# Kernel optimization log

Measured on AMD Instinct MI355X. Metric: run time of the kernel, lower is better.

Reference implementation:

```python
import jax, jax.numpy as jnp
import numpy as np

C = 64; NB_ERB = 32; NB_DF = 96; EMB = 256; KT = 2
LSNR_SCALE = 50.0; LSNR_OFFSET = -15.0

def _conv2d(x, w, b, stride=(1, 1)):
    # NCHW conv; freq padding 1, no temporal padding (causal ring buffer handles time)
    out = jax.lax.conv_general_dilated(
        x, w, window_strides=stride, padding=((0, 0), (1, 1)),
        dimension_numbers=('NCHW', 'OIHW', 'NCHW'))
    return out + b[None, :, None, None]


def setup_inputs() -> dict:
    key = jax.random.key(0)
    ks = jax.random.split(key, 32)
    n = lambda i, shape, s=0.05: jax.random.normal(ks[i], shape, dtype=jnp.float32) * s
    return {
        'feat_erb': n(0, (1, 1, 1, NB_ERB), 1.0),
        'feat_spec': n(1, (1, 2, 1, NB_DF), 1.0),
        'buf_erb0': n(2, (1, 1, KT - 1, NB_ERB), 1.0),
        'buf_df0': n(3, (1, 2, KT - 1, NB_DF), 1.0),
        'h_enc': n(4, (1, 1, EMB), 1.0),
        'W_erb0': n(5, (C, 1, KT, 3)), 'b_erb0': n(6, (C,)),
        'W_erb1': n(7, (C, C, 1, 3)), 'b_erb1': n(8, (C,)),
        'W_erb2': n(9, (C, C, 1, 3)), 'b_erb2': n(10, (C,)),
        'W_erb3': n(11, (C, C, 1, 3)), 'b_erb3': n(12, (C,)),
        'W_df0': n(13, (C, 2, KT, 3)), 'b_df0': n(14, (C,)),
        'W_df1': n(15, (C, C, 1, 3)), 'b_df1': n(16, (C,)),
        'W_dffc': n(17, (EMB, C * (NB_DF // 2))), 'b_dffc': n(18, (EMB,)),
        'W_ih': n(19, (3 * EMB, EMB)), 'b_ih': n(20, (3 * EMB,)),
        'W_hh': n(21, (3 * EMB, EMB)), 'b_hh': n(22, (3 * EMB,)),
        'W_lsnr': n(23, (1, EMB)), 'b_lsnr': n(24, (1,)),
    }


def reference(feat_erb, feat_spec, buf_erb0, buf_df0, h_enc,
              W_erb0, b_erb0, W_erb1, b_erb1, W_erb2, b_erb2, W_erb3, b_erb3,
              W_df0, b_df0, W_df1, b_df1, W_dffc, b_dffc,
              W_ih, b_ih, W_hh, b_hh, W_lsnr, b_lsnr):
    relu = jax.nn.relu
    # ERB path: causal conv via explicit ring buffer
    ctx_erb = jnp.concatenate([buf_erb0, feat_erb], axis=2)     # [1,1,KT,32]
    e0 = relu(_conv2d(ctx_erb, W_erb0, b_erb0))                 # [1,C,1,32]
    buf_erb0_new = ctx_erb[:, :, 1:, :]
    e1 = relu(_conv2d(e0, W_erb1, b_erb1, stride=(1, 2)))       # [1,C,1,16]
    e2 = relu(_conv2d(e1, W_erb2, b_erb2, stride=(1, 2)))       # [1,C,1,8]
    e3 = relu(_conv2d(e2, W_erb3, b_erb3, stride=(1, 2)))       # [1,C,1,4]
    # DF path
    ctx_df = jnp.concatenate([buf_df0, feat_spec], axis=2)      # [1,2,KT,96]
    c0 = relu(_conv2d(ctx_df, W_df0, b_df0))                    # [1,C,1,96]
    buf_df0_new = ctx_df[:, :, 1:, :]
    c1 = relu(_conv2d(c0, W_df1, b_df1, stride=(1, 2)))         # [1,C,1,48]
    c1f = jnp.transpose(c1, (0, 2, 3, 1)).reshape(1, 1, -1)     # [1,1,48*C]
    cemb = relu(c1f @ W_dffc.T + b_dffc)                        # [1,1,EMB]
    emb_raw = jnp.transpose(e3, (0, 2, 3, 1)).reshape(1, 1, -1) # [1,1,EMB]
    emb_raw = emb_raw + cemb                                    # combine = add
    # Single-layer GRU step (torch gate semantics)
    x2 = emb_raw[:, 0]                                          # [1,EMB]
    h2 = h_enc[0]                                               # [1,EMB]
    gi = x2 @ W_ih.T + b_ih
    gh = h2 @ W_hh.T + b_hh
    ir, iz, inn = jnp.split(gi, 3, axis=-1)
    hr, hz, hn = jnp.split(gh, 3, axis=-1)
    r = jax.nn.sigmoid(ir + hr)
    z = jax.nn.sigmoid(iz + hz)
    ng = jnp.tanh(inn + r * hn)
    h_new = (1.0 - z) * ng + z * h2                             # [1,EMB]
    emb = h_new[:, None, :]                                     # [1,1,EMB]
    h_enc_new = h_new[None]                                     # [1,1,EMB]
    lsnr = (jax.nn.sigmoid(emb @ W_lsnr.T + b_lsnr) * LSNR_SCALE + LSNR_OFFSET).reshape(1)
    return (e0, e1, e2, e3, emb, c0, lsnr, buf_erb0_new, buf_df0_new, h_enc_new)
```

## Files before the change

### kernel.cpp

```cpp
#include <hip/hip_runtime.h>
#include <math.h>

#define C 64
#define NB_ERB 32
#define NB_DF 96
#define EMB 256

#define OUT_E0      0
#define OUT_E1      2048
#define OUT_E2      3072
#define OUT_E3      3584
#define OUT_EMB     3840
#define OUT_C0      4096
#define OUT_LSNR    10240
#define OUT_BUF_ERB 10241
#define OUT_BUF_DF  10273
#define OUT_HENC    10465

#define WS_GH   0
#define WS_PART 768

static __device__ __forceinline__ float sigm(float x) {
    return 1.0f / (1.0f + expf(-x));
}

__global__ __launch_bounds__(256) void k1(
    const float* __restrict__ feat_erb, const float* __restrict__ feat_spec,
    const float* __restrict__ buf_erb0, const float* __restrict__ buf_df0,
    const float* __restrict__ h_enc,
    const float* __restrict__ W_erb0, const float* __restrict__ b_erb0,
    const float* __restrict__ W_df0,  const float* __restrict__ b_df0,
    const float* __restrict__ W_hh,   const float* __restrict__ b_hh,
    float* __restrict__ out, float* __restrict__ ws)
{
    const int blk = blockIdx.x, t = threadIdx.x;
    if (blk < 24) {
        int g = blk * 256 + t;
        int o = g / NB_DF, w = g % NB_DF;
        float acc = b_df0[o];
        const float* W = W_df0 + o * 12;
        #pragma unroll
        for (int c = 0; c < 2; ++c)
            #pragma unroll
            for (int kw = 0; kw < 3; ++kw) {
                int x = w + kw - 1;
                if (x >= 0 && x < NB_DF) {
                    acc += W[c * 6 + kw]     * buf_df0[c * NB_DF + x];
                    acc += W[c * 6 + 3 + kw] * feat_spec[c * NB_DF + x];
                }
            }
        out[OUT_C0 + g] = fmaxf(acc, 0.0f);
    } else if (blk < 32) {
        int g = (blk - 24) * 256 + t;
        int o = g / NB_ERB, w = g % NB_ERB;
        float acc = b_erb0[o];
        const float* W = W_erb0 + o * 6;
        #pragma unroll
        for (int kw = 0; kw < 3; ++kw) {
            int x = w + kw - 1;
            if (x >= 0 && x < NB_ERB) {
                acc += W[kw]     * buf_erb0[x];
                acc += W[3 + kw] * feat_erb[x];
            }
        }
        out[OUT_E0 + g] = fmaxf(acc, 0.0f);
    } else if (blk < 224) {
        int o = (blk - 32) * 4 + (t >> 6);
        int lane = t & 63;
        const float4 wv = *reinterpret_cast<const float4*>(W_hh + o * EMB + lane * 4);
        const float4 hv = *reinterpret_cast<const float4*>(h_enc + lane * 4);
        float a = wv.x * hv.x + wv.y * hv.y + wv.z * hv.z + wv.w * hv.w;
        #pragma unroll
        for (int off = 32; off; off >>= 1) a += __shfl_down(a, off);
        if (lane == 0) ws[WS_GH + o] = a + b_hh[o];
    } else {
        if (t < 32)  out[OUT_BUF_ERB + t] = feat_erb[t];
        if (t < 192) out[OUT_BUF_DF + t]  = feat_spec[t];
    }
}

__global__ __launch_bounds__(256) void k2(
    const float* __restrict__ W_erb1, const float* __restrict__ b_erb1,
    const float* __restrict__ W_erb2, const float* __restrict__ b_erb2,
    const float* __restrict__ W_erb3, const float* __restrict__ b_erb3,
    const float* __restrict__ W_df1,  const float* __restrict__ b_df1,
    const float* __restrict__ W_dffc,
    float* __restrict__ out, float* __restrict__ ws)
{
    const int blk = blockIdx.x, t = threadIdx.x;
    if (blk == 0) {
        __shared__ float sW[64 * 193];
        __shared__ float sA[2048];
        __shared__ float sB[1024];

        for (int k = t; k < 2048; k += 256) sA[k] = out[OUT_E0 + k];
        for (int k = t; k < 12288; k += 256) sW[(k / 192) * 193 + (k % 192)] = W_erb1[k];
        __syncthreads();

        const int o = t & 63, wg = t >> 6;
        {
            float a0 = b_erb1[o], a1 = a0, a2 = a0, a3 = a0;
            for (int i = 0; i < 64; ++i) {
                float w0 = sW[o * 193 + i * 3 + 0];
                float w1 = sW[o * 193 + i * 3 + 1];
                float w2 = sW[o * 193 + i * 3 + 2];
                const float* e = &sA[i * 32];
                int xb = wg * 8 - 1;
                float ev[9];
                #pragma unroll
                for (int m = 0; m < 9; ++m) {
                    int x = xb + m;
                    ev[m] = (x >= 0) ? e[x] : 0.0f;
                }
                a0 += w0 * ev[0] + w1 * ev[1] + w2 * ev[2];
                a1 += w0 * ev[2] + w1 * ev[3] + w2 * ev[4];
                a2 += w0 * ev[4] + w1 * ev[5] + w2 * ev[6];
                a3 += w0 * ev[6] + w1 * ev[7] + w2 * ev[8];
            }
            a0 = fmaxf(a0, 0.0f); a1 = fmaxf(a1, 0.0f);
            a2 = fmaxf(a2, 0.0f); a3 = fmaxf(a3, 0.0f);
            int w = wg * 4;
            out[OUT_E1 + o * 16 + w + 0] = a0; sB[o * 16 + w + 0] = a0;
            out[OUT_E1 + o * 16 + w + 1] = a1; sB[o * 16 + w + 1] = a1;
            out[OUT_E1 + o * 16 + w + 2] = a2; sB[o * 16 + w + 2] = a2;
            out[OUT_E1 + o * 16 + w + 3] = a3; sB[o * 16 + w + 3] = a3;
        }
        __syncthreads();
        for (int k = t; k < 12288; k += 256) sW[(k / 192) * 193 + (k % 192)] = W_erb2[k];
        __syncthreads();

        {
            float a0 = b_erb2[o], a1 = a0;
            for (int i = 0; i < 64; ++i) {
                float w0 = sW[o * 193 + i * 3 + 0];
                float w1 = sW[o * 193 + i * 3 + 1];
                float w2 = sW[o * 193 + i * 3 + 2];
                const float* e = &sB[i * 16];
                int xb = 4 * wg - 1;
                float v0 = (xb >= 0) ? e[xb] : 0.0f;
                float v1 = e[xb + 1], v2 = e[xb + 2], v3 = e[xb + 3], v4 = e[xb + 4];
                a0 += w0 * v0 + w1 * v1 + w2 * v2;
                a1 += w0 * v2 + w1 * v3 + w2 * v4;
            }
            a0 = fmaxf(a0, 0.0f); a1 = fmaxf(a1, 0.0f);
            __syncthreads();
            int w = 2 * wg;
            out[OUT_E2 + o * 8 + w + 0] = a0; sA[o * 8 + w + 0] = a0;
            out[OUT_E2 + o * 8 + w + 1] = a1; sA[o * 8 + w + 1] = a1;
        }
        __syncthreads();
        for (int k = t; k < 12288; k += 256) sW[(k / 192) * 193 + (k % 192)] = W_erb3[k];
        __syncthreads();

        {
            float a = b_erb3[o];
            for (int i = 0; i < 64; ++i) {
                float w0 = sW[o * 193 + i * 3 + 0];
                float w1 = sW[o * 193 + i * 3 + 1];
                float w2 = sW[o * 193 + i * 3 + 2];
                const float* e = &sA[i * 8];
                int xb = 2 * wg - 1;
                float v0 = (xb >= 0) ? e[xb] : 0.0f;
                a += w0 * v0 + w1 * e[xb + 1] + w2 * e[xb + 2];
            }
            out[OUT_E3 + o * 4 + wg] = fmaxf(a, 0.0f);
        }
    } else {
        const int w = blk - 1;
        __shared__ float s_c1[64];
        const int c = t >> 2, p = t & 3;
        float acc = 0.0f;
        const float* c0p = out + OUT_C0;
        for (int ii = 0; ii < 16; ++ii) {
            int i = p * 16 + ii;
            const float* Wr = W_df1 + c * 192 + i * 3;
            const float* cr = c0p + i * NB_DF;
            #pragma unroll
            for (int kw = 0; kw < 3; ++kw) {
                int x = 2 * w + kw - 1;
                if (x >= 0) acc += Wr[kw] * cr[x];
            }
        }
        acc += __shfl_down(acc, 2, 4);
        acc += __shfl_down(acc, 1, 4);
        if (p == 0) s_c1[c] = fmaxf(acc + b_df1[c], 0.0f);
        __syncthreads();
        {
            const float4* Wp = reinterpret_cast<const float4*>(W_dffc + t * 3072 + w * 64);
            float a = 0.0f;
            #pragma unroll
            for (int q = 0; q < 16; ++q) {
                float4 v = Wp[q];
                a += v.x * s_c1[q * 4 + 0] + v.y * s_c1[q * 4 + 1]
                   + v.z * s_c1[q * 4 + 2] + v.w * s_c1[q * 4 + 3];
            }
            ws[WS_PART + w * 256 + t] = a;
        }
    }
}

__global__ __launch_bounds__(1024) void k3(
    const float* __restrict__ h_enc, const float* __restrict__ b_dffc,
    const float* __restrict__ W_ih,  const float* __restrict__ b_ih,
    const float* __restrict__ W_lsnr, const float* __restrict__ b_lsnr,
    float* __restrict__ out, float* __restrict__ ws)
{
    const int t = threadIdx.x;
    __shared__ __align__(16) float s_x2[256];
    __shared__ float s_h2[256];
    __shared__ float s_gi[768];
    __shared__ float s_hn[256];

    if (t < 256) {
        float acc = b_dffc[t];
        for (int w = 0; w < 48; ++w) acc += ws[WS_PART + w * 256 + t];
        float cemb = fmaxf(acc, 0.0f);
        float e3v = out[OUT_E3 + (t & 63) * 4 + (t >> 6)];
        s_x2[t] = e3v + cemb;
        s_h2[t] = h_enc[t];
    }
    __syncthreads();

    const int wv = t >> 6, lane = t & 63;
    const float4 xv = *reinterpret_cast<const float4*>(&s_x2[lane * 4]);
    for (int o = wv; o < 256; o += 16) {
        const float4 wr = *reinterpret_cast<const float4*>(W_ih + (o      ) * 256 + lane * 4);
        const float4 wz = *reinterpret_cast<const float4*>(W_ih + (o + 256) * 256 + lane * 4);
        const float4 wn = *reinterpret_cast<const float4*>(W_ih + (o + 512) * 256 + lane * 4);
        float ar = wr.x * xv.x + wr.y * xv.y + wr.z * xv.z + wr.w * xv.w;
        float az = wz.x * xv.x + wz.y * xv.y + wz.z * xv.z + wz.w * xv.w;
        float an = wn.x * xv.x + wn.y * xv.y + wn.z * xv.z + wn.w * xv.w;
        #pragma unroll
        for (int off = 32; off; off >>= 1) {
            ar += __shfl_down(ar, off);
            az += __shfl_down(az, off);
            an += __shfl_down(an, off);
        }
        if (lane == 0) {
            s_gi[o      ] = ar + b_ih[o      ];
            s_gi[o + 256] = az + b_ih[o + 256];
            s_gi[o + 512] = an + b_ih[o + 512];
        }
    }
    __syncthreads();

    if (t < 256) {
        float r  = sigm(s_gi[t      ] + ws[WS_GH + t      ]);
        float z  = sigm(s_gi[256 + t] + ws[WS_GH + 256 + t]);
        float ng = tanhf(s_gi[512 + t] + r * ws[WS_GH + 512 + t]);
        float h  = (1.0f - z) * ng + z * s_h2[t];
        out[OUT_EMB  + t] = h;
        out[OUT_HENC + t] = h;
        s_hn[t] = h * W_lsnr[t];
    }
    __syncthreads();

    if (t < 64) {
        float a = s_hn[t] + s_hn[64 + t] + s_hn[128 + t] + s_hn[192 + t];
        #pragma unroll
        for (int off = 32; off; off >>= 1) a += __shfl_down(a, off);
        if (t == 0)
            out[OUT_LSNR] = sigm(a + b_lsnr[0]) * 50.0f - 15.0f;
    }
}

extern "C" void kernel_launch(void* const* d_in, const int* in_sizes, int n_in,
                              void* d_out, int out_size, void* d_ws, size_t ws_size,
                              hipStream_t stream) {
    (void)in_sizes; (void)n_in; (void)out_size; (void)ws_size;
    const float* feat_erb  = (const float*)d_in[0];
    const float* feat_spec = (const float*)d_in[1];
    const float* buf_erb0  = (const float*)d_in[2];
    const float* buf_df0   = (const float*)d_in[3];
    const float* h_enc     = (const float*)d_in[4];
    const float* W_erb0    = (const float*)d_in[5];
    const float* b_erb0    = (const float*)d_in[6];
    const float* W_erb1    = (const float*)d_in[7];
    const float* b_erb1    = (const float*)d_in[8];
    const float* W_erb2    = (const float*)d_in[9];
    const float* b_erb2    = (const float*)d_in[10];
    const float* W_erb3    = (const float*)d_in[11];
    const float* b_erb3    = (const float*)d_in[12];
    const float* W_df0     = (const float*)d_in[13];
    const float* b_df0     = (const float*)d_in[14];
    const float* W_df1     = (const float*)d_in[15];
    const float* b_df1     = (const float*)d_in[16];
    const float* W_dffc    = (const float*)d_in[17];
    const float* b_dffc    = (const float*)d_in[18];
    const float* W_ih      = (const float*)d_in[19];
    const float* b_ih      = (const float*)d_in[20];
    const float* W_hh      = (const float*)d_in[21];
    const float* b_hh      = (const float*)d_in[22];
    const float* W_lsnr    = (const float*)d_in[23];
    const float* b_lsnr    = (const float*)d_in[24];
    float* out = (float*)d_out;
    float* ws  = (float*)d_ws;

    hipLaunchKernelGGL(k1, dim3(225), dim3(256), 0, stream,
                       feat_erb, feat_spec, buf_erb0, buf_df0, h_enc,
                       W_erb0, b_erb0, W_df0, b_df0, W_hh, b_hh, out, ws);
    hipLaunchKernelGGL(k2, dim3(49), dim3(256), 0, stream,
                       W_erb1, b_erb1, W_erb2, b_erb2, W_erb3, b_erb3,
                       W_df1, b_df1, W_dffc, out, ws);
    hipLaunchKernelGGL(k3, dim3(1), dim3(1024), 0, stream,
                       h_enc, b_dffc, W_ih, b_ih, W_lsnr, b_lsnr, out, ws);
}
```

Before: 144.3 us.

## Spread GRU input matvec across blocks, prefetch conv weights, cache DF inputs in shared memory

```diff
diff --git a/kernel.cpp b/kernel.cpp
--- a/kernel.cpp
+++ b/kernel.cpp
@@ -1,7 +1,6 @@
 #include <hip/hip_runtime.h>
 #include <math.h>
 
-#define C 64
 #define NB_ERB 32
 #define NB_DF 96
 #define EMB 256
@@ -64,15 +63,25 @@
             }
         }
         out[OUT_E0 + g] = fmaxf(acc, 0.0f);
-    } else if (blk < 224) {
-        int o = (blk - 32) * 4 + (t >> 6);
-        int lane = t & 63;
-        const float4 wv = *reinterpret_cast<const float4*>(W_hh + o * EMB + lane * 4);
+    } else if (blk < 80) {
+        const int wv = t >> 6, lane = t & 63;
+        const int o0 = (blk - 32) * 16 + wv * 4;
         const float4 hv = *reinterpret_cast<const float4*>(h_enc + lane * 4);
-        float a = wv.x * hv.x + wv.y * hv.y + wv.z * hv.z + wv.w * hv.w;
-        #pragma unroll
-        for (int off = 32; off; off >>= 1) a += __shfl_down(a, off);
-        if (lane == 0) ws[WS_GH + o] = a + b_hh[o];
+        float r[4];
+        #pragma unroll
+        for (int j = 0; j < 4; ++j) {
+            const float4 wr = *reinterpret_cast<const float4*>(W_hh + (o0 + j) * EMB + lane * 4);
+            r[j] = wr.x * hv.x + wr.y * hv.y + wr.z * hv.z + wr.w * hv.w;
+        }
+        #pragma unroll
+        for (int off = 32; off; off >>= 1) {
+            #pragma unroll
+            for (int j = 0; j < 4; ++j) r[j] += __shfl_down(r[j], off);
+        }
+        if (lane == 0) {
+            #pragma unroll
+            for (int j = 0; j < 4; ++j) ws[WS_GH + o0 + j] = r[j] + b_hh[o0 + j];
+        }
     } else {
         if (t < 32)  out[OUT_BUF_ERB + t] = feat_erb[t];
         if (t < 192) out[OUT_BUF_DF + t]  = feat_spec[t];
@@ -88,98 +97,134 @@
     float* __restrict__ out, float* __restrict__ ws)
 {
     const int blk = blockIdx.x, t = threadIdx.x;
+    __shared__ float sW1[64 * 193];
+    __shared__ float sW2[64 * 193];
+    __shared__ __align__(16) float sA[2048];
+    __shared__ __align__(16) float sB[1024];
+    __shared__ float s_c0[192];
+    __shared__ float s_c1[64];
+
     if (blk == 0) {
-        __shared__ float sW[64 * 193];
-        __shared__ float sA[2048];
-        __shared__ float sB[1024];
-
-        for (int k = t; k < 2048; k += 256) sA[k] = out[OUT_E0 + k];
-        for (int k = t; k < 12288; k += 256) sW[(k / 192) * 193 + (k % 192)] = W_erb1[k];
-        __syncthreads();
-
         const int o = t & 63, wg = t >> 6;
-        {
-            float a0 = b_erb1[o], a1 = a0, a2 = a0, a3 = a0;
+        float4 wbuf[12];
+
+        {
+            const float4* W1v = reinterpret_cast<const float4*>(W_erb1);
+            #pragma unroll
+            for (int j = 0; j < 12; ++j) wbuf[j] = W1v[t + 256 * j];
+            const float4* e0v = reinterpret_cast<const float4*>(out + OUT_E0);
+            float4 a0 = e0v[t], a1 = e0v[t + 256];
+            reinterpret_cast<float4*>(sA)[t]       = a0;
+            reinterpret_cast<float4*>(sA)[t + 256] = a1;
+            #pragma unroll
+            for (int j = 0; j < 12; ++j) {
+                int k4 = t + 256 * j;
+                float* p = &sW1[(k4 / 48) * 193 + (k4 % 48) * 4];
+                p[0] = wbuf[j].x; p[1] = wbuf[j].y; p[2] = wbuf[j].z; p[3] = wbuf[j].w;
+            }
+            const float4* W2v = reinterpret_cast<const float4*>(W_erb2);
+            #pragma unroll
+            for (int j = 0; j < 12; ++j) wbuf[j] = W2v[t + 256 * j];
+        }
+        __syncthreads();
+
+        {
+            float bias = b_erb1[o];
+            float a0 = bias, a1 = bias, a2 = bias, a3 = bias;
+            const float* wrow = &sW1[o * 193];
             for (int i = 0; i < 64; ++i) {
-                float w0 = sW[o * 193 + i * 3 + 0];
-                float w1 = sW[o * 193 + i * 3 + 1];
-                float w2 = sW[o * 193 + i * 3 + 2];
-                const float* e = &sA[i * 32];
-                int xb = wg * 8 - 1;
-                float ev[9];
-                #pragma unroll
-                for (int m = 0; m < 9; ++m) {
-                    int x = xb + m;
-                    ev[m] = (x >= 0) ? e[x] : 0.0f;
-                }
-                a0 += w0 * ev[0] + w1 * ev[1] + w2 * ev[2];
-                a1 += w0 * ev[2] + w1 * ev[3] + w2 * ev[4];
-                a2 += w0 * ev[4] + w1 * ev[5] + w2 * ev[6];
-                a3 += w0 * ev[6] + w1 * ev[7] + w2 * ev[8];
+                float w0 = wrow[i * 3], w1 = wrow[i * 3 + 1], w2 = wrow[i * 3 + 2];
+                const float* e = &sA[i * 32 + wg * 8];
+                float em1 = (wg == 0) ? 0.0f : e[-1];
+                float4 v0 = *reinterpret_cast<const float4*>(e);
+                float4 v1 = *reinterpret_cast<const float4*>(e + 4);
+                a0 += w0 * em1  + w1 * v0.x + w2 * v0.y;
+                a1 += w0 * v0.y + w1 * v0.z + w2 * v0.w;
+                a2 += w0 * v0.w + w1 * v1.x + w2 * v1.y;
+                a3 += w0 * v1.y + w1 * v1.z + w2 * v1.w;
+            }
+            float4 r = make_float4(fmaxf(a0, 0.f), fmaxf(a1, 0.f),
+                                   fmaxf(a2, 0.f), fmaxf(a3, 0.f));
+            reinterpret_cast<float4*>(&sB[o * 16])[wg] = r;
+            reinterpret_cast<float4*>(out + OUT_E1)[o * 4 + wg] = r;
+        }
+        {
+            #pragma unroll
+            for (int j = 0; j < 12; ++j) {
+                int k4 = t + 256 * j;
+                float* p = &sW2[(k4 / 48) * 193 + (k4 % 48) * 4];
+                p[0] = wbuf[j].x; p[1] = wbuf[j].y; p[2] = wbuf[j].z; p[3] = wbuf[j].w;
+            }
+            const float4* W3v = reinterpret_cast<const float4*>(W_erb3);
+            #pragma unroll
+            for (int j = 0; j < 12; ++j) wbuf[j] = W3v[t + 256 * j];
+        }
+        __syncthreads();
+
+        {
+            float bias = b_erb2[o];
+            float a0 = bias, a1 = bias;
+            const float* wrow = &sW2[o * 193];
+            for (int i = 0; i < 64; ++i) {
+                float w0 = wrow[i * 3], w1 = wrow[i * 3 + 1], w2 = wrow[i * 3 + 2];
+                const float* e = &sB[i * 16 + wg * 4];
+                float em1 = (wg == 0) ? 0.0f : e[-1];
+                float4 v = *reinterpret_cast<const float4*>(e);
+                a0 += w0 * em1 + w1 * v.x + w2 * v.y;
+                a1 += w0 * v.y + w1 * v.z + w2 * v.w;
             }
             a0 = fmaxf(a0, 0.0f); a1 = fmaxf(a1, 0.0f);
-            a2 = fmaxf(a2, 0.0f); a3 = fmaxf(a3, 0.0f);
-            int w = wg * 4;
-            out[OUT_E1 + o * 16 + w + 0] = a0; sB[o * 16 + w + 0] = a0;
-            out[OUT_E1 + o * 16 + w + 1] = a1; sB[o * 16 + w + 1] = a1;
-            out[OUT_E1 + o * 16 + w + 2] = a2; sB[o * 16 + w + 2] = a2;
-            out[OUT_E1 + o * 16 + w + 3] = a3; sB[o * 16 + w + 3] = a3;
-        }
-        __syncthreads();
-        for (int k = t; k < 12288; k += 256) sW[(k / 192) * 193 + (k % 192)] = W_erb2[k];
-        __syncthreads();
-
-        {
-            float a0 = b_erb2[o], a1 = a0;
+            int w = 2 * wg;
+            sA[o * 8 + w] = a0; sA[o * 8 + w + 1] = a1;
+            out[OUT_E2 + o * 8 + w] = a0; out[OUT_E2 + o * 8 + w + 1] = a1;
+        }
+        {
+            #pragma unroll
+            for (int j = 0; j < 12; ++j) {
+                int k4 = t + 256 * j;
+                float* p = &sW1[(k4 / 48) * 193 + (k4 % 48) * 4];
+                p[0] = wbuf[j].x; p[1] = wbuf[j].y; p[2] = wbuf[j].z; p[3] = wbuf[j].w;
+            }
+        }
+        __syncthreads();
+
+        {
+            float a = b_erb3[o];
+            const float* wrow = &sW1[o * 193];
             for (int i = 0; i < 64; ++i) {
-                float w0 = sW[o * 193 + i * 3 + 0];
-                float w1 = sW[o * 193 + i * 3 + 1];
-                float w2 = sW[o * 193 + i * 3 + 2];
-                const float* e = &sB[i * 16];
-                int xb = 4 * wg - 1;
-                float v0 = (xb >= 0) ? e[xb] : 0.0f;
-                float v1 = e[xb + 1], v2 = e[xb + 2], v3 = e[xb + 3], v4 = e[xb + 4];
-                a0 += w0 * v0 + w1 * v1 + w2 * v2;
-                a1 += w0 * v2 + w1 * v3 + w2 * v4;
-            }
-            a0 = fmaxf(a0, 0.0f); a1 = fmaxf(a1, 0.0f);
-            __syncthreads();
-            int w = 2 * wg;
-            out[OUT_E2 + o * 8 + w + 0] = a0; sA[o * 8 + w + 0] = a0;
-            out[OUT_E2 + o * 8 + w + 1] = a1; sA[o * 8 + w + 1] = a1;
-        }
-        __syncthreads();
-        for (int k = t; k < 12288; k += 256) sW[(k / 192) * 193 + (k % 192)] = W_erb3[k];
-        __syncthreads();
-
-        {
-            float a = b_erb3[o];
-            for (int i = 0; i < 64; ++i) {
-                float w0 = sW[o * 193 + i * 3 + 0];
-                float w1 = sW[o * 193 + i * 3 + 1];
-                float w2 = sW[o * 193 + i * 3 + 2];
-                const float* e = &sA[i * 8];
-                int xb = 2 * wg - 1;
-                float v0 = (xb >= 0) ? e[xb] : 0.0f;
-                a += w0 * v0 + w1 * e[xb + 1] + w2 * e[xb + 2];
+                float w0 = wrow[i * 3], w1 = wrow[i * 3 + 1], w2 = wrow[i * 3 + 2];
+                const float* e = &sA[i * 8 + 2 * wg];
+                float em1 = (wg == 0) ? 0.0f : e[-1];
+                a += w0 * em1 + w1 * e[0] + w2 * e[1];
             }
             out[OUT_E3 + o * 4 + wg] = fmaxf(a, 0.0f);
         }
     } else {
         const int w = blk - 1;
-        __shared__ float s_c1[64];
+        const float* c0p = out + OUT_C0;
+        if (t < 192) {
+            int i = t / 3, kw = t % 3, x = 2 * w + kw - 1;
+            s_c0[t] = (x >= 0) ? c0p[i * NB_DF + x] : 0.0f;
+        }
+        __syncthreads();
         const int c = t >> 2, p = t & 3;
+        float wloc[48];
+        {
+            const float4* Wv = reinterpret_cast<const float4*>(W_df1 + c * 192 + p * 48);
+            #pragma unroll
+            for (int q = 0; q < 12; ++q) {
+                float4 v = Wv[q];
+                wloc[4 * q] = v.x; wloc[4 * q + 1] = v.y;
+                wloc[4 * q + 2] = v.z; wloc[4 * q + 3] = v.w;
+            }
+        }
         float acc = 0.0f;
-        const float* c0p = out + OUT_C0;
+        #pragma unroll
         for (int ii = 0; ii < 16; ++ii) {
             int i = p * 16 + ii;
-            const float* Wr = W_df1 + c * 192 + i * 3;
-            const float* cr = c0p + i * NB_DF;
-            #pragma unroll
-            for (int kw = 0; kw < 3; ++kw) {
-                int x = 2 * w + kw - 1;
-                if (x >= 0) acc += Wr[kw] * cr[x];
-            }
+            acc += wloc[ii * 3]     * s_c0[i * 3]
+                 + wloc[ii * 3 + 1] * s_c0[i * 3 + 1]
+                 + wloc[ii * 3 + 2] * s_c0[i * 3 + 2];
         }
         acc += __shfl_down(acc, 2, 4);
         acc += __shfl_down(acc, 1, 4);
@@ -191,7 +236,7 @@
             #pragma unroll
             for (int q = 0; q < 16; ++q) {
                 float4 v = Wp[q];
-                a += v.x * s_c1[q * 4 + 0] + v.y * s_c1[q * 4 + 1]
+                a += v.x * s_c1[q * 4]     + v.y * s_c1[q * 4 + 1]
                    + v.z * s_c1[q * 4 + 2] + v.w * s_c1[q * 4 + 3];
             }
             ws[WS_PART + w * 256 + t] = a;
@@ -199,69 +244,60 @@
     }
 }
 
-__global__ __launch_bounds__(1024) void k3(
+__global__ __launch_bounds__(256) void k3(
     const float* __restrict__ h_enc, const float* __restrict__ b_dffc,
     const float* __restrict__ W_ih,  const float* __restrict__ b_ih,
-    const float* __restrict__ W_lsnr, const float* __restrict__ b_lsnr,
     float* __restrict__ out, float* __restrict__ ws)
 {
-    const int t = threadIdx.x;
+    const int t = threadIdx.x, blk = blockIdx.x;
     __shared__ __align__(16) float s_x2[256];
-    __shared__ float s_h2[256];
-    __shared__ float s_gi[768];
-    __shared__ float s_hn[256];
-
-    if (t < 256) {
+    {
         float acc = b_dffc[t];
+        #pragma unroll 8
         for (int w = 0; w < 48; ++w) acc += ws[WS_PART + w * 256 + t];
         float cemb = fmaxf(acc, 0.0f);
         float e3v = out[OUT_E3 + (t & 63) * 4 + (t >> 6)];
         s_x2[t] = e3v + cemb;
-        s_h2[t] = h_enc[t];
     }
     __syncthreads();
-
     const int wv = t >> 6, lane = t & 63;
+    const int o = blk * 4 + wv;
     const float4 xv = *reinterpret_cast<const float4*>(&s_x2[lane * 4]);
-    for (int o = wv; o < 256; o += 16) {
-        const float4 wr = *reinterpret_cast<const float4*>(W_ih + (o      ) * 256 + lane * 4);
-        const float4 wz = *reinterpret_cast<const float4*>(W_ih + (o + 256) * 256 + lane * 4);
-        const float4 wn = *reinterpret_cast<const float4*>(W_ih + (o + 512) * 256 + lane * 4);
-        float ar = wr.x * xv.x + wr.y * xv.y + wr.z * xv.z + wr.w * xv.w;
-        float az = wz.x * xv.x + wz.y * xv.y + wz.z * xv.z + wz.w * xv.w;
-        float an = wn.x * xv.x + wn.y * xv.y + wn.z * xv.z + wn.w * xv.w;
-        #pragma unroll
-        for (int off = 32; off; off >>= 1) {
-            ar += __shfl_down(ar, off);
-            az += __shfl_down(az, off);
-            an += __shfl_down(an, off);
-        }
-        if (lane == 0) {
-            s_gi[o      ] = ar + b_ih[o      ];
-            s_gi[o + 256] = az + b_ih[o + 256];
-            s_gi[o + 512] = an + b_ih[o + 512];
-        }
-    }
+    const float4 wr = *reinterpret_cast<const float4*>(W_ih + (o      ) * EMB + lane * 4);
+    const float4 wz = *reinterpret_cast<const float4*>(W_ih + (o + 256) * EMB + lane * 4);
+    const float4 wn = *reinterpret_cast<const float4*>(W_ih + (o + 512) * EMB + lane * 4);
+    float ar = wr.x * xv.x + wr.y * xv.y + wr.z * xv.z + wr.w * xv.w;
+    float az = wz.x * xv.x + wz.y * xv.y + wz.z * xv.z + wz.w * xv.w;
+    float an = wn.x * xv.x + wn.y * xv.y + wn.z * xv.z + wn.w * xv.w;
+    #pragma unroll
+    for (int off = 32; off; off >>= 1) {
+        ar += __shfl_down(ar, off);
+        az += __shfl_down(az, off);
+        an += __shfl_down(an, off);
+    }
+    if (lane == 0) {
+        float r  = sigm(ar + b_ih[o]       + ws[WS_GH + o]);
+        float z  = sigm(az + b_ih[o + 256] + ws[WS_GH + 256 + o]);
+        float ng = tanhf(an + b_ih[o + 512] + r * ws[WS_GH + 512 + o]);
+        float h  = (1.0f - z) * ng + z * h_enc[o];
+        out[OUT_EMB  + o] = h;
+        out[OUT_HENC + o] = h;
+    }
+}
+
+__global__ __launch_bounds__(256) void k4(
+    const float* __restrict__ W_lsnr, const float* __restrict__ b_lsnr,
+    float* __restrict__ out)
+{
+    const int t = threadIdx.x;
+    __shared__ float s[4];
+    float v = out[OUT_EMB + t] * W_lsnr[t];
+    #pragma unroll
+    for (int off = 32; off; off >>= 1) v += __shfl_down(v, off);
+    if ((t & 63) == 0) s[t >> 6] = v;
     __syncthreads();
-
-    if (t < 256) {
-        float r  = sigm(s_gi[t      ] + ws[WS_GH + t      ]);
-        float z  = sigm(s_gi[256 + t] + ws[WS_GH + 256 + t]);
-        float ng = tanhf(s_gi[512 + t] + r * ws[WS_GH + 512 + t]);
-        float h  = (1.0f - z) * ng + z * s_h2[t];
-        out[OUT_EMB  + t] = h;
-        out[OUT_HENC + t] = h;
-        s_hn[t] = h * W_lsnr[t];
-    }
-    __syncthreads();
-
-    if (t < 64) {
-        float a = s_hn[t] + s_hn[64 + t] + s_hn[128 + t] + s_hn[192 + t];
-        #pragma unroll
-        for (int off = 32; off; off >>= 1) a += __shfl_down(a, off);
-        if (t == 0)
-            out[OUT_LSNR] = sigm(a + b_lsnr[0]) * 50.0f - 15.0f;
-    }
+    if (t == 0)
+        out[OUT_LSNR] = sigm(s[0] + s[1] + s[2] + s[3] + b_lsnr[0]) * 50.0f - 15.0f;
 }
 
 extern "C" void kernel_launch(void* const* d_in, const int* in_sizes, int n_in,
@@ -296,12 +332,14 @@
     float* out = (float*)d_out;
     float* ws  = (float*)d_ws;
 
-    hipLaunchKernelGGL(k1, dim3(225), dim3(256), 0, stream,
+    hipLaunchKernelGGL(k1, dim3(81), dim3(256), 0, stream,
                        feat_erb, feat_spec, buf_erb0, buf_df0, h_enc,
                        W_erb0, b_erb0, W_df0, b_df0, W_hh, b_hh, out, ws);
     hipLaunchKernelGGL(k2, dim3(49), dim3(256), 0, stream,
                        W_erb1, b_erb1, W_erb2, b_erb2, W_erb3, b_erb3,
                        W_df1, b_df1, W_dffc, out, ws);
-    hipLaunchKernelGGL(k3, dim3(1), dim3(1024), 0, stream,
-                       h_enc, b_dffc, W_ih, b_ih, W_lsnr, b_lsnr, out, ws);
-}
+    hipLaunchKernelGGL(k3, dim3(64), dim3(256), 0, stream,
+                       h_enc, b_dffc, W_ih, b_ih, out, ws);
+    hipLaunchKernelGGL(k4, dim3(1), dim3(256), 0, stream,
+                       W_lsnr, b_lsnr, out);
+}
```

Result: faster. 126.0 us (-12.7%).
